# Kernel optimization log

Hardware: AMD Instinct MI355X
Metric: run time of the kernel (lower is better)

Reference implementation:

```python
import jax, jax.numpy as jnp
import numpy as np

B, S, D = 32, 4096, 512

def setup_inputs() -> dict:
    key = jax.random.key(0)
    ks = jax.random.split(key, 5)
    scale = 1.0 / np.sqrt(D)
    return {
        "query": jax.random.normal(ks[0], (B, D), jnp.float32),
        "values": jax.random.normal(ks[1], (B, S, D), jnp.float32),
        "W1": jax.random.normal(ks[2], (D, D), jnp.float32) * scale,
        "b1": jnp.zeros((D,), jnp.float32),
        "W2": jax.random.normal(ks[3], (D, D), jnp.float32) * scale,
        "b2": jnp.zeros((D,), jnp.float32),
        "V": jax.random.normal(ks[4], (D, 1), jnp.float32) * scale,
        "bv": jnp.zeros((1,), jnp.float32),
    }

def reference(query, values, W1, b1, W2, b2, V, bv):
    # query: [B, D], values: [B, S, D]
    q_proj = query @ W1 + b1                      # [B, D]
    v_proj = jnp.einsum('bsd,de->bse', values, W2) + b2  # [B, S, D]
    hidden = jnp.tanh(q_proj[:, None, :] + v_proj)       # [B, S, D]
    score = jnp.einsum('bsd,de->bse', hidden, V) + bv    # [B, S, 1]
    attn = jax.nn.softmax(score, axis=1)                 # softmax over seq axis
    context = jnp.sum(attn * values, axis=1)             # [B, D]
    return (context, attn)
```

## Files before the change

kernel.cpp:

```cpp
#include <hip/hip_runtime.h>
#include <hip/hip_bf16.h>
#include <stdint.h>

#define NB 32
#define NS 4096
#define ND 512

typedef __attribute__((ext_vector_type(8))) short short8;
typedef __attribute__((ext_vector_type(4))) float floatx4;

__device__ __forceinline__ short f2bf(float f) {
    unsigned int u = __builtin_bit_cast(unsigned int, f);
    return (short)((u + 0x8000u) >> 16);
}

__device__ __forceinline__ float fast_tanh(float x) {
    float e = __expf(2.0f * x);
    return 1.0f - 2.0f * __builtin_amdgcn_rcpf(e + 1.0f);
}

__global__ void __launch_bounds__(256) qproj_kernel(
    const float* __restrict__ query, const float* __restrict__ W1,
    const float* __restrict__ b1, const float* __restrict__ b2,
    float* __restrict__ qb) {
    const int b  = blockIdx.x;
    const int es = blockIdx.y;
    const int t  = threadIdx.x;
    const int col = t & 63, kc = t >> 6;
    __shared__ float q[ND];
    __shared__ float red[256];
    q[t] = query[b * ND + t];
    q[t + 256] = query[b * ND + t + 256];
    __syncthreads();
    float acc = 0.f;
    const float* wp = W1 + (size_t)(kc * 128) * ND + es * 64 + col;
    const float* qp = q + kc * 128;
#pragma unroll 8
    for (int k = 0; k < 128; k++)
        acc += qp[k] * wp[(size_t)k * ND];
    red[t] = acc;
    __syncthreads();
    if (t < 64) {
        float s = red[t] + red[t + 64] + red[t + 128] + red[t + 192];
        int e = es * 64 + t;
        qb[b * ND + e] = s + b1[e] + b2[e];
    }
}

__global__ void __launch_bounds__(256) w2t_kernel(
    const float* __restrict__ W2, unsigned short* __restrict__ W2Tt) {
    int g = blockIdx.x * 256 + threadIdx.x;
    int nt = g >> 14;
    int ks = (g >> 10) & 15;
    int kq = (g >> 8) & 3;
    int n  = g & 255;
    int e  = nt * 256 + n;
    int k0 = ks * 32 + kq * 8;
    short8 v;
#pragma unroll
    for (int j = 0; j < 8; j++)
        v[j] = f2bf(W2[(size_t)(k0 + j) * ND + e]);
    *(short8*)&W2Tt[(size_t)g * 8] = v;
}

__global__ void __launch_bounds__(256, 3) scores_kernel(
    const float* __restrict__ values, const unsigned short* __restrict__ W2Tt,
    const float* __restrict__ qb, const float* __restrict__ V,
    float* __restrict__ scores) {
    const int nt = blockIdx.x;
    const int st = blockIdx.y;
    const int b  = blockIdx.z;
    const int n0 = nt * 256, s0 = st * 64;

    __shared__ __align__(16) float sA[2][2048];
    __shared__ __align__(16) unsigned short sB[2][8192];
    __shared__ float sQb[256];
    __shared__ float sV[256];

    const int tid  = threadIdx.x;
    const int lane = tid & 63;
    const int wave = tid >> 6;
    const int mr = lane & 15;
    const int q  = lane >> 4;

    sQb[tid] = qb[b * ND + n0 + tid];
    sV[tid]  = V[n0 + tid];

    floatx4 acc[4][4] = {};

    const float* abase = values + ((size_t)b * NS + s0) * ND;
    const unsigned short* bbase = W2Tt + (size_t)(nt * 16) * 8192;

#pragma unroll
    for (int r = 0; r < 4; r++) {
        int c = tid + 256 * r;
        __builtin_amdgcn_global_load_lds(
            (const __attribute__((address_space(1))) unsigned int*)(bbase + c * 8),
            (__attribute__((address_space(3))) unsigned int*)&sB[0][c * 8],
            16, 0, 0);
    }
#pragma unroll
    for (int r = 0; r < 2; r++) {
        int c = tid + 256 * r;
        int row = c >> 3;
        int kq4 = (c & 7) ^ (row & 7);
        __builtin_amdgcn_global_load_lds(
            (const __attribute__((address_space(1))) unsigned int*)(abase + (size_t)row * ND + kq4 * 4),
            (__attribute__((address_space(3))) unsigned int*)&sA[0][c * 4],
            16, 0, 0);
    }
    __syncthreads();

    for (int ks = 0; ks < 16; ks++) {
        const int cur = ks & 1, nxt = cur ^ 1;

        short8 af[4], bfr[4];
#pragma unroll
        for (int i = 0; i < 4; i++) {
            int row = i * 16 + mr;
            int c0 = row * 8 + ((2 * q) ^ (mr & 7));
            float4 f0 = *(const float4*)&sA[cur][c0 * 4];
            float4 f1 = *(const float4*)&sA[cur][(c0 ^ 1) * 4];
            short8 a;
            a[0] = f2bf(f0.x); a[1] = f2bf(f0.y); a[2] = f2bf(f0.z); a[3] = f2bf(f0.w);
            a[4] = f2bf(f1.x); a[5] = f2bf(f1.y); a[6] = f2bf(f1.z); a[7] = f2bf(f1.w);
            af[i] = a;
        }
#pragma unroll
        for (int j = 0; j < 4; j++)
            bfr[j] = *(const short8*)&sB[cur][(q * 256 + wave * 64 + j * 16 + mr) * 8];

        if (ks < 15) {
            const unsigned short* bsrc = bbase + (size_t)(ks + 1) * 8192;
            const float* asrc = abase + (ks + 1) * 32;
#pragma unroll
            for (int r = 0; r < 4; r++) {
                int c = tid + 256 * r;
                __builtin_amdgcn_global_load_lds(
                    (const __attribute__((address_space(1))) unsigned int*)(bsrc + c * 8),
                    (__attribute__((address_space(3))) unsigned int*)&sB[nxt][c * 8],
                    16, 0, 0);
            }
#pragma unroll
            for (int r = 0; r < 2; r++) {
                int c = tid + 256 * r;
                int row = c >> 3;
                int kq4 = (c & 7) ^ (row & 7);
                __builtin_amdgcn_global_load_lds(
                    (const __attribute__((address_space(1))) unsigned int*)(asrc + (size_t)row * ND + kq4 * 4),
                    (__attribute__((address_space(3))) unsigned int*)&sA[nxt][c * 4],
                    16, 0, 0);
            }
        }

#pragma unroll
        for (int i = 0; i < 4; i++)
#pragma unroll
            for (int j = 0; j < 4; j++)
                acc[i][j] = __builtin_amdgcn_mfma_f32_16x16x32_bf16(af[i], bfr[j], acc[i][j], 0, 0, 0);

        __syncthreads();
    }

    float vcoef[4], qadd[4];
#pragma unroll
    for (int j = 0; j < 4; j++) {
        int col = wave * 64 + j * 16 + mr;
        vcoef[j] = sV[col];
        qadd[j]  = sQb[col];
    }

#pragma unroll
    for (int i = 0; i < 4; i++) {
#pragma unroll
        for (int r = 0; r < 4; r++) {
            float p = 0.f;
#pragma unroll
            for (int j = 0; j < 4; j++)
                p += fast_tanh(acc[i][j][r] + qadd[j]) * vcoef[j];
            p += __shfl_xor(p, 1);
            p += __shfl_xor(p, 2);
            p += __shfl_xor(p, 4);
            p += __shfl_xor(p, 8);
            if (mr == 0) {
                int row = i * 16 + q * 4 + r;
                atomicAdd(&scores[(size_t)b * NS + s0 + row], p);
            }
        }
    }
}

__global__ void __launch_bounds__(256) softmax_kernel(
    const float* __restrict__ scores, float* __restrict__ attn) {
    int b = blockIdx.x;
    int t = threadIdx.x;
    __shared__ float red[4];
    __shared__ float bcast[2];
    const float* sc = scores + (size_t)b * NS;
    float v[16];
    float m = -1e30f;
#pragma unroll
    for (int i = 0; i < 16; i++) { v[i] = sc[t + i * 256]; m = fmaxf(m, v[i]); }
    for (int o = 32; o; o >>= 1) m = fmaxf(m, __shfl_xor(m, o));
    if ((t & 63) == 0) red[t >> 6] = m;
    __syncthreads();
    if (t == 0) bcast[0] = fmaxf(fmaxf(red[0], red[1]), fmaxf(red[2], red[3]));
    __syncthreads();
    m = bcast[0];
    float sum = 0.f;
#pragma unroll
    for (int i = 0; i < 16; i++) { v[i] = __expf(v[i] - m); sum += v[i]; }
    for (int o = 32; o; o >>= 1) sum += __shfl_xor(sum, o);
    if ((t & 63) == 0) red[t >> 6] = sum;
    __syncthreads();
    if (t == 0) bcast[1] = red[0] + red[1] + red[2] + red[3];
    __syncthreads();
    float inv = 1.0f / bcast[1];
    float* ao = attn + (size_t)b * NS;
#pragma unroll
    for (int i = 0; i < 16; i++) ao[t + i * 256] = v[i] * inv;
}

__global__ void __launch_bounds__(256) context_partial_kernel(
    const float* __restrict__ values, const float* __restrict__ attn,
    float* __restrict__ pctx) {
    int sc = blockIdx.x;
    int b  = blockIdx.y;
    int t  = threadIdx.x;
    __shared__ float sAttn[512];
    sAttn[t]       = attn[(size_t)b * NS + sc * 512 + t];
    sAttn[t + 256] = attn[(size_t)b * NS + sc * 512 + t + 256];
    __syncthreads();
    int d = t * 2;
    const float2* vp = (const float2*)(values + ((size_t)b * NS + sc * 512) * ND + d);
    float ax = 0.f, ay = 0.f;
#pragma unroll 8
    for (int s = 0; s < 512; s++) {
        float a = sAttn[s];
        float2 v = vp[(size_t)s * 256];
        ax += a * v.x; ay += a * v.y;
    }
    pctx[((size_t)sc * 32 + b) * ND + d]     = ax;
    pctx[((size_t)sc * 32 + b) * ND + d + 1] = ay;
}

__global__ void __launch_bounds__(256) context_reduce_kernel(
    const float* __restrict__ pctx, float* __restrict__ ctx) {
    int i = blockIdx.x * 256 + threadIdx.x;
    float s = 0.f;
#pragma unroll
    for (int p = 0; p < 8; p++) s += pctx[(size_t)p * (32 * ND) + i];
    ctx[i] = s;
}

extern "C" void kernel_launch(void* const* d_in, const int* in_sizes, int n_in,
                              void* d_out, int out_size, void* d_ws, size_t ws_size,
                              hipStream_t stream) {
    const float* query  = (const float*)d_in[0];
    const float* values = (const float*)d_in[1];
    const float* W1     = (const float*)d_in[2];
    const float* b1     = (const float*)d_in[3];
    const float* W2     = (const float*)d_in[4];
    const float* b2     = (const float*)d_in[5];
    const float* V      = (const float*)d_in[6];

    float* ctx_out  = (float*)d_out;
    float* attn_out = (float*)d_out + NB * ND;

    char* ws = (char*)d_ws;
    float*          qb     = (float*)ws;
    unsigned short* W2Tt   = (unsigned short*)(ws + (64 << 10));
    float*          scores = (float*)(ws + (64 << 10) + (512 << 10));
    float*          pctx   = (float*)(ws + (64 << 10) + (1024 << 10));

    hipMemsetAsync(scores, 0, (size_t)NB * NS * sizeof(float), stream);

    qproj_kernel<<<dim3(NB, 8), 256, 0, stream>>>(query, W1, b1, b2, qb);
    w2t_kernel<<<128, 256, 0, stream>>>(W2, W2Tt);
    scores_kernel<<<dim3(2, 64, 32), 256, 0, stream>>>(values, W2Tt, qb, V, scores);
    softmax_kernel<<<NB, 256, 0, stream>>>(scores, attn_out);
    context_partial_kernel<<<dim3(8, 32), 256, 0, stream>>>(values, attn_out, pctx);
    context_reduce_kernel<<<64, 256, 0, stream>>>(pctx, ctx_out);
}
```

Before: 498.0 us.

## Register-prefetch and pre-convert A tile to bf16, drop atomics and memset

The values tile is now loaded into registers two k-steps ahead, converted to bf16 with packed conversion instructions, and written to LDS once. The MFMA loop then reads bf16 fragments directly instead of reconverting fp32 data in every wave. Score atomics are replaced by an in-block LDS reduction that writes per-N-tile partials, which the softmax sums, so the memset is no longer needed. The context partial kernel splits the sequence into twice as many chunks for more parallelism, and pctx reuses the pscores workspace. This adds register pressure and relies on inline asm.

```diff
diff --git a/kernel.cpp b/kernel.cpp
--- a/kernel.cpp
+++ b/kernel.cpp
@@ -8,10 +8,17 @@
 
 typedef __attribute__((ext_vector_type(8))) short short8;
 typedef __attribute__((ext_vector_type(4))) float floatx4;
+typedef __attribute__((ext_vector_type(4))) unsigned int uint4v;
 
 __device__ __forceinline__ short f2bf(float f) {
     unsigned int u = __builtin_bit_cast(unsigned int, f);
     return (short)((u + 0x8000u) >> 16);
+}
+
+__device__ __forceinline__ unsigned int cvt_pk_bf16(float lo, float hi) {
+    unsigned int r;
+    asm("v_cvt_pk_bf16_f32 %0, %1, %2" : "=v"(r) : "v"(lo), "v"(hi));
+    return r;
 }
 
 __device__ __forceinline__ float fast_tanh(float x) {
@@ -66,16 +73,17 @@
 __global__ void __launch_bounds__(256, 3) scores_kernel(
     const float* __restrict__ values, const unsigned short* __restrict__ W2Tt,
     const float* __restrict__ qb, const float* __restrict__ V,
-    float* __restrict__ scores) {
+    float* __restrict__ pscores) {
     const int nt = blockIdx.x;
     const int st = blockIdx.y;
     const int b  = blockIdx.z;
     const int n0 = nt * 256, s0 = st * 64;
 
-    __shared__ __align__(16) float sA[2][2048];
+    __shared__ __align__(16) unsigned short sA[2][2048];
     __shared__ __align__(16) unsigned short sB[2][8192];
     __shared__ float sQb[256];
     __shared__ float sV[256];
+    __shared__ float sRed[4][64];
 
     const int tid  = threadIdx.x;
     const int lane = tid & 63;
@@ -88,9 +96,19 @@
 
     floatx4 acc[4][4] = {};
 
-    const float* abase = values + ((size_t)b * NS + s0) * ND;
+    const int arow = tid >> 2;
+    const int ac   = tid & 3;
+    const int ardo = arow * 32 + ((ac ^ ((tid >> 3) & 3)) * 8);
+    const float* ag = values + ((size_t)b * NS + s0 + arow) * ND + ac * 8;
+
+    const int afo = (q ^ ((mr >> 1) & 3)) * 8;
+
     const unsigned short* bbase = W2Tt + (size_t)(nt * 16) * 8192;
 
+    float4 p0 = *(const float4*)(ag);
+    float4 p1 = *(const float4*)(ag + 4);
+    float4 arA0 = *(const float4*)(ag + 32);
+    float4 arA1 = *(const float4*)(ag + 36);
 #pragma unroll
     for (int r = 0; r < 4; r++) {
         int c = tid + 256 * r;
@@ -99,40 +117,28 @@
             (__attribute__((address_space(3))) unsigned int*)&sB[0][c * 8],
             16, 0, 0);
     }
-#pragma unroll
-    for (int r = 0; r < 2; r++) {
-        int c = tid + 256 * r;
-        int row = c >> 3;
-        int kq4 = (c & 7) ^ (row & 7);
-        __builtin_amdgcn_global_load_lds(
-            (const __attribute__((address_space(1))) unsigned int*)(abase + (size_t)row * ND + kq4 * 4),
-            (__attribute__((address_space(3))) unsigned int*)&sA[0][c * 4],
-            16, 0, 0);
-    }
-    __syncthreads();
-
+    {
+        uint4v w;
+        w.x = cvt_pk_bf16(p0.x, p0.y); w.y = cvt_pk_bf16(p0.z, p0.w);
+        w.z = cvt_pk_bf16(p1.x, p1.y); w.w = cvt_pk_bf16(p1.z, p1.w);
+        *(uint4v*)&sA[0][ardo] = w;
+    }
+    __syncthreads();
+
+#pragma unroll
     for (int ks = 0; ks < 16; ks++) {
         const int cur = ks & 1, nxt = cur ^ 1;
 
         short8 af[4], bfr[4];
 #pragma unroll
-        for (int i = 0; i < 4; i++) {
-            int row = i * 16 + mr;
-            int c0 = row * 8 + ((2 * q) ^ (mr & 7));
-            float4 f0 = *(const float4*)&sA[cur][c0 * 4];
-            float4 f1 = *(const float4*)&sA[cur][(c0 ^ 1) * 4];
-            short8 a;
-            a[0] = f2bf(f0.x); a[1] = f2bf(f0.y); a[2] = f2bf(f0.z); a[3] = f2bf(f0.w);
-            a[4] = f2bf(f1.x); a[5] = f2bf(f1.y); a[6] = f2bf(f1.z); a[7] = f2bf(f1.w);
-            af[i] = a;
-        }
+        for (int i = 0; i < 4; i++)
+            af[i] = *(const short8*)&sA[cur][(i * 16 + mr) * 32 + afo];
 #pragma unroll
         for (int j = 0; j < 4; j++)
             bfr[j] = *(const short8*)&sB[cur][(q * 256 + wave * 64 + j * 16 + mr) * 8];
 
         if (ks < 15) {
             const unsigned short* bsrc = bbase + (size_t)(ks + 1) * 8192;
-            const float* asrc = abase + (ks + 1) * 32;
 #pragma unroll
             for (int r = 0; r < 4; r++) {
                 int c = tid + 256 * r;
@@ -141,16 +147,11 @@
                     (__attribute__((address_space(3))) unsigned int*)&sB[nxt][c * 8],
                     16, 0, 0);
             }
-#pragma unroll
-            for (int r = 0; r < 2; r++) {
-                int c = tid + 256 * r;
-                int row = c >> 3;
-                int kq4 = (c & 7) ^ (row & 7);
-                __builtin_amdgcn_global_load_lds(
-                    (const __attribute__((address_space(1))) unsigned int*)(asrc + (size_t)row * ND + kq4 * 4),
-                    (__attribute__((address_space(3))) unsigned int*)&sA[nxt][c * 4],
-                    16, 0, 0);
-            }
+        }
+        float4 n0v = {}, n1v = {};
+        if (ks < 14) {
+            n0v = *(const float4*)(ag + (ks + 2) * 32);
+            n1v = *(const float4*)(ag + (ks + 2) * 32 + 4);
         }
 
 #pragma unroll
@@ -158,6 +159,14 @@
 #pragma unroll
             for (int j = 0; j < 4; j++)
                 acc[i][j] = __builtin_amdgcn_mfma_f32_16x16x32_bf16(af[i], bfr[j], acc[i][j], 0, 0, 0);
+
+        if (ks < 15) {
+            uint4v w;
+            w.x = cvt_pk_bf16(arA0.x, arA0.y); w.y = cvt_pk_bf16(arA0.z, arA0.w);
+            w.z = cvt_pk_bf16(arA1.x, arA1.y); w.w = cvt_pk_bf16(arA1.z, arA1.w);
+            *(uint4v*)&sA[nxt][ardo] = w;
+        }
+        arA0 = n0v; arA1 = n1v;
 
         __syncthreads();
     }
@@ -182,25 +191,31 @@
             p += __shfl_xor(p, 2);
             p += __shfl_xor(p, 4);
             p += __shfl_xor(p, 8);
-            if (mr == 0) {
-                int row = i * 16 + q * 4 + r;
-                atomicAdd(&scores[(size_t)b * NS + s0 + row], p);
-            }
-        }
+            if (mr == 0) sRed[wave][i * 16 + q * 4 + r] = p;
+        }
+    }
+    __syncthreads();
+    if (tid < 64) {
+        float s = sRed[0][tid] + sRed[1][tid] + sRed[2][tid] + sRed[3][tid];
+        pscores[((size_t)nt * NB + b) * NS + s0 + tid] = s;
     }
 }
 
 __global__ void __launch_bounds__(256) softmax_kernel(
-    const float* __restrict__ scores, float* __restrict__ attn) {
+    const float* __restrict__ pscores, float* __restrict__ attn) {
     int b = blockIdx.x;
     int t = threadIdx.x;
     __shared__ float red[4];
     __shared__ float bcast[2];
-    const float* sc = scores + (size_t)b * NS;
+    const float* sc0 = pscores + (size_t)b * NS;
+    const float* sc1 = pscores + (size_t)(NB + b) * NS;
     float v[16];
     float m = -1e30f;
 #pragma unroll
-    for (int i = 0; i < 16; i++) { v[i] = sc[t + i * 256]; m = fmaxf(m, v[i]); }
+    for (int i = 0; i < 16; i++) {
+        v[i] = sc0[t + i * 256] + sc1[t + i * 256];
+        m = fmaxf(m, v[i]);
+    }
     for (int o = 32; o; o >>= 1) m = fmaxf(m, __shfl_xor(m, o));
     if ((t & 63) == 0) red[t >> 6] = m;
     __syncthreads();
@@ -227,15 +242,14 @@
     int sc = blockIdx.x;
     int b  = blockIdx.y;
     int t  = threadIdx.x;
-    __shared__ float sAttn[512];
-    sAttn[t]       = attn[(size_t)b * NS + sc * 512 + t];
-    sAttn[t + 256] = attn[(size_t)b * NS + sc * 512 + t + 256];
+    __shared__ float sAttn[256];
+    sAttn[t] = attn[(size_t)b * NS + sc * 256 + t];
     __syncthreads();
     int d = t * 2;
-    const float2* vp = (const float2*)(values + ((size_t)b * NS + sc * 512) * ND + d);
+    const float2* vp = (const float2*)(values + ((size_t)b * NS + sc * 256) * ND + d);
     float ax = 0.f, ay = 0.f;
 #pragma unroll 8
-    for (int s = 0; s < 512; s++) {
+    for (int s = 0; s < 256; s++) {
         float a = sAttn[s];
         float2 v = vp[(size_t)s * 256];
         ax += a * v.x; ay += a * v.y;
@@ -249,7 +263,7 @@
     int i = blockIdx.x * 256 + threadIdx.x;
     float s = 0.f;
 #pragma unroll
-    for (int p = 0; p < 8; p++) s += pctx[(size_t)p * (32 * ND) + i];
+    for (int p = 0; p < 16; p++) s += pctx[(size_t)p * (32 * ND) + i];
     ctx[i] = s;
 }
 
@@ -268,17 +282,15 @@
     float* attn_out = (float*)d_out + NB * ND;
 
     char* ws = (char*)d_ws;
-    float*          qb     = (float*)ws;
-    unsigned short* W2Tt   = (unsigned short*)(ws + (64 << 10));
-    float*          scores = (float*)(ws + (64 << 10) + (512 << 10));
-    float*          pctx   = (float*)(ws + (64 << 10) + (1024 << 10));
-
-    hipMemsetAsync(scores, 0, (size_t)NB * NS * sizeof(float), stream);
+    float*          qb      = (float*)ws;
+    unsigned short* W2Tt    = (unsigned short*)(ws + (64 << 10));
+    float*          pscores = (float*)(ws + (576 << 10));
+    float*          pctx    = pscores;
 
     qproj_kernel<<<dim3(NB, 8), 256, 0, stream>>>(query, W1, b1, b2, qb);
     w2t_kernel<<<128, 256, 0, stream>>>(W2, W2Tt);
-    scores_kernel<<<dim3(2, 64, 32), 256, 0, stream>>>(values, W2Tt, qb, V, scores);
-    softmax_kernel<<<NB, 256, 0, stream>>>(scores, attn_out);
-    context_partial_kernel<<<dim3(8, 32), 256, 0, stream>>>(values, attn_out, pctx);
+    scores_kernel<<<dim3(2, 64, 32), 256, 0, stream>>>(values, W2Tt, qb, V, pscores);
+    softmax_kernel<<<NB, 256, 0, stream>>>(pscores, attn_out);
+    context_partial_kernel<<<dim3(16, 32), 256, 0, stream>>>(values, attn_out, pctx);
     context_reduce_kernel<<<64, 256, 0, stream>>>(pctx, ctx_out);
 }
```

After: 487.6 us. -2.1%, faster.
